# Kernel optimization log

Hardware: AMD Instinct MI355X
Metric: run time of the kernel (lower is better)

Reference implementation:

```python
import jax, jax.numpy as jnp
import numpy as np

N, E = 50000, 600000
IN_DIM, HID, HYP = 384, 128, 256
NUM_LAYERS = 3
TAU = 0.5
ALPHA = 0.1
EPS = 1e-10


def setup_inputs() -> dict:
    keys = jax.random.split(jax.random.key(0), 10)
    x = jax.random.normal(keys[0], (N, IN_DIM), dtype=jnp.float32)
    edge_index = jax.random.randint(keys[1], (2, E), 0, N, dtype=jnp.int32)
    gumbel_u = jax.random.uniform(keys[2], (N, HYP), dtype=jnp.float32, minval=1e-6, maxval=1.0 - 1e-6)
    # parameters (xavier-ish scaling)
    w_feat = jax.random.normal(keys[3], (IN_DIM, HID), dtype=jnp.float32) * np.float32(1.0 / np.sqrt(IN_DIM))
    b_feat = jnp.zeros((HID,), jnp.float32)
    w_hyper = jax.random.normal(keys[4], (HID, HYP), dtype=jnp.float32) * np.float32(np.sqrt(2.0 / (HID + HYP)))
    w_vis = jax.random.normal(keys[5], (HID, HID), dtype=jnp.float32) * np.float32(1.0 / np.sqrt(HID))
    b_vis = jnp.zeros((HID,), jnp.float32)
    w_txt = jax.random.normal(keys[6], (HID, HID), dtype=jnp.float32) * np.float32(1.0 / np.sqrt(HID))
    b_txt = jnp.zeros((HID,), jnp.float32)
    return {"x": x, "edge_index": edge_index, "gumbel_u": gumbel_u,
            "w_feat": w_feat, "b_feat": b_feat, "w_hyper": w_hyper,
            "w_vis": w_vis, "b_vis": b_vis, "w_txt": w_txt, "b_txt": b_txt}


def reference(x, edge_index, gumbel_u, w_feat, b_feat, w_hyper, w_vis, b_vis, w_txt, b_txt):
    src, dst = edge_index[0], edge_index[1]
    # LGConv gcn_norm (no self loops): deg from in-edges, norm = d_src^-1/2 * d_dst^-1/2
    deg = jax.ops.segment_sum(jnp.ones((E,), x.dtype), dst, num_segments=N)
    dinv = jnp.where(deg > 0, jnp.where(deg > 0, deg, 1.0) ** -0.5, 0.0)
    ew = dinv[src] * dinv[dst]  # [E]

    x_emb = x @ w_feat + b_feat  # [N, HID] (dropout p=0 / eval: identity)

    # stacked LightGCN propagation, mean over (num_layers+1) layer outputs
    acc = x_emb
    cur = x_emb
    for _ in range(NUM_LAYERS):
        cur = jax.ops.segment_sum(cur[src] * ew[:, None], dst, num_segments=N)
        acc = acc + cur
    local = acc / jnp.asarray(NUM_LAYERS + 1, x.dtype)

    # HGNN: gumbel-softmax soft assignment + two dense matmuls
    logits = x_emb @ w_hyper  # [N, HYP]
    g = -jnp.log(-jnp.log(gumbel_u + EPS) + EPS)
    Hm = jax.nn.softmax((logits + g) / TAU, axis=1)  # [N, HYP]
    lat = Hm.T @ x_emb            # [HYP, HID]
    hyper_out = Hm @ lat          # [N, HID]

    # F.normalize(p=2, dim=1) with eps clamp 1e-12
    nrm = jnp.maximum(jnp.linalg.norm(hyper_out, axis=1, keepdims=True), 1e-12)
    final = local + ALPHA * (hyper_out / nrm)

    x_vision = jax.nn.relu(final @ w_vis + b_vis)
    x_text = jax.nn.relu(final @ w_txt + b_txt)
    return final, x_vision, x_text
```

## Files before the change

### kernel.cpp

```cpp
#include <hip/hip_runtime.h>
#include <math.h>

#define N_NODES 50000
#define E_EDGES 600000
#define IN_DIM  384
#define HID     128
#define HYP     256

#define SCAN_NB ((N_NODES + 255) / 256)
#define EMB_NB  (N_NODES / 16)
#define DEG_NB  ((E_EDGES + 255) / 256)

#define XS_STRIDE 392

typedef __attribute__((ext_vector_type(8))) short bf16x8;
typedef __attribute__((ext_vector_type(4))) float f32x4;
typedef _Float16 f16x4 __attribute__((ext_vector_type(4)));
typedef _Float16 f16x8 __attribute__((ext_vector_type(8)));

__device__ __forceinline__ unsigned short f2bf(float f) {
    unsigned u = __builtin_bit_cast(unsigned, f);
    u = (u + 0x7FFFu + ((u >> 16) & 1u)) >> 16;
    return (unsigned short)u;
}

__device__ __forceinline__ bf16x8 cvt8(float4 p, float4 q) {
    bf16x8 a;
    a[0] = (short)f2bf(p.x); a[1] = (short)f2bf(p.y);
    a[2] = (short)f2bf(p.z); a[3] = (short)f2bf(p.w);
    a[4] = (short)f2bf(q.x); a[5] = (short)f2bf(q.y);
    a[6] = (short)f2bf(q.z); a[7] = (short)f2bf(q.w);
    return a;
}

__device__ __forceinline__ bf16x8 cvt8h(f16x8 h) {
    bf16x8 a;
#pragma unroll
    for (int i = 0; i < 8; ++i) a[i] = (short)f2bf((float)h[i]);
    return a;
}


__global__ __launch_bounds__(256) void k_scan1(const int* __restrict__ deg, int* __restrict__ bsum) {
    __shared__ int sh[256];
    int tid = threadIdx.x;
    int i = blockIdx.x * 256 + tid;
    sh[tid] = (i < N_NODES) ? deg[i] : 0;
    __syncthreads();
#pragma unroll
    for (int off = 128; off > 0; off >>= 1) {
        if (tid < off) sh[tid] += sh[tid + off];
        __syncthreads();
    }
    if (tid == 0) bsum[blockIdx.x] = sh[0];
}

__global__ __launch_bounds__(256) void k_scan2(const int* __restrict__ bsum, int* __restrict__ bbase,
                                               int* __restrict__ row_start) {
    __shared__ int sh[256];
    int tid = threadIdx.x;
    int v = (tid < SCAN_NB) ? bsum[tid] : 0;
    sh[tid] = v;
    __syncthreads();
#pragma unroll
    for (int off = 1; off < 256; off <<= 1) {
        int t = (tid >= off) ? sh[tid - off] : 0;
        __syncthreads();
        sh[tid] += t;
        __syncthreads();
    }
    if (tid < SCAN_NB) bbase[tid] = sh[tid] - v;
    if (tid == 0) row_start[N_NODES] = E_EDGES;
}

__global__ __launch_bounds__(256) void k_scan3(const int* __restrict__ deg, const int* __restrict__ bbase,
                                               int* __restrict__ row_start, float* __restrict__ dinv) {
    __shared__ int sh[256];
    int tid = threadIdx.x;
    int i = blockIdx.x * 256 + tid;
    int d = (i < N_NODES) ? deg[i] : 0;
    sh[tid] = d;
    __syncthreads();
#pragma unroll
    for (int off = 1; off < 256; off <<= 1) {
        int t = (tid >= off) ? sh[tid - off] : 0;
        __syncthreads();
        sh[tid] += t;
        __syncthreads();
    }
    if (i < N_NODES) {
        row_start[i] = sh[tid] - d + bbase[blockIdx.x];
        dinv[i] = (d > 0) ? rsqrtf((float)d) : 0.0f;
    }
}

__global__ void k_fill(const int* __restrict__ src, const int* __restrict__ dst,
                       const int* __restrict__ row_start, int* __restrict__ cnt,
                       const float* __restrict__ dinv, int2* __restrict__ csr_sw) {
    int i = blockIdx.x * blockDim.x + threadIdx.x;
    if (i < E_EDGES) {
        int d = dst[i], s = src[i];
        int pos = row_start[d] + atomicAdd(&cnt[d], 1);
        csr_sw[pos] = make_int2(s, __float_as_int(dinv[s] * dinv[d]));
    }
}


__global__ __launch_bounds__(256) void k_cvt_all(const float* __restrict__ wf, const float* __restrict__ wh,
                                                 const float* __restrict__ wv, const float* __restrict__ wt,
                                                 unsigned short* __restrict__ wfT, unsigned short* __restrict__ whT,
                                                 unsigned short* __restrict__ wvT, unsigned short* __restrict__ wtT) {
    int i = blockIdx.x * 256 + threadIdx.x;
    if (i < 49152) {
        int r = i >> 7, c = i & 127;
        wfT[(size_t)c * IN_DIM + r] = f2bf(wf[i]);
    } else if (i < 49152 + 32768) {
        int j = i - 49152;
        int r = j >> 8, c = j & 255;
        whT[(size_t)c * HID + r] = f2bf(wh[j]);
    } else if (i < 49152 + 32768 + 16384) {
        int j = i - 81920;
        int r = j >> 7, c = j & 127;
        wvT[(size_t)c * HID + r] = f2bf(wv[j]);
    } else {
        int j = i - 98304;
        int r = j >> 7, c = j & 127;
        wtT[(size_t)c * HID + r] = f2bf(wt[j]);
    }
}


__global__ __launch_bounds__(256) void k_embdeg(const float* __restrict__ x, const unsigned short* __restrict__ wfT,
                                                const float* __restrict__ bf_, _Float16* __restrict__ x_embh,
                                                const int* __restrict__ dst, int* __restrict__ deg) {
    int b = blockIdx.x;
    int tid = threadIdx.x;
    if (b >= EMB_NB) {
        int i = (b - EMB_NB) * 256 + tid;
        if (i < E_EDGES) atomicAdd(&deg[dst[i]], 1);
        return;
    }
    __shared__ unsigned short xs[16 * XS_STRIDE];
    int m0 = b * 16;
    const float* xbase = x + (size_t)m0 * IN_DIM;
#pragma unroll
    for (int pass = 0; pass < 6; ++pass) {
        int j = pass * 256 + tid;
        int row = (j * 683) >> 16;
        int col = (j - row * 96) * 4;
        float4 v = *reinterpret_cast<const float4*>(xbase + (size_t)row * IN_DIM + col);
        ushort4 sv = make_ushort4(f2bf(v.x), f2bf(v.y), f2bf(v.z), f2bf(v.w));
        *reinterpret_cast<ushort4*>(&xs[row * XS_STRIDE + col]) = sv;
    }
    __syncthreads();
    int wave = tid >> 6;
    int lane = tid & 63;
    int l16 = lane & 15, quad = lane >> 4;
    int c0 = wave * 32;
    const unsigned short* wp0 = wfT + (size_t)(c0 + l16) * IN_DIM + quad * 8;
    const unsigned short* wp1 = wp0 + (size_t)16 * IN_DIM;
    f32x4 acc0 = (f32x4){0.f, 0.f, 0.f, 0.f};
    f32x4 acc1 = (f32x4){0.f, 0.f, 0.f, 0.f};
#pragma unroll
    for (int kt = 0; kt < 12; ++kt) {
        bf16x8 a = *reinterpret_cast<const bf16x8*>(&xs[l16 * XS_STRIDE + kt * 32 + quad * 8]);
        bf16x8 b0 = *reinterpret_cast<const bf16x8*>(wp0 + kt * 32);
        bf16x8 b1 = *reinterpret_cast<const bf16x8*>(wp1 + kt * 32);
        acc0 = __builtin_amdgcn_mfma_f32_16x16x32_bf16(a, b0, acc0, 0, 0, 0);
        acc1 = __builtin_amdgcn_mfma_f32_16x16x32_bf16(a, b1, acc1, 0, 0, 0);
    }
    float bias0 = bf_[c0 + l16];
    float bias1 = bf_[c0 + 16 + l16];
#pragma unroll
    for (int r = 0; r < 4; ++r) {
        size_t row = (size_t)(m0 + quad * 4 + r);
        x_embh[row * HID + c0 + l16]      = (_Float16)(acc0[r] + bias0);
        x_embh[row * HID + c0 + 16 + l16] = (_Float16)(acc1[r] + bias1);
    }
}


__device__ __forceinline__ void fma4h(float4& a, const f16x4 v, float s) {
    a.x = fmaf((float)v.x, s, a.x);
    a.y = fmaf((float)v.y, s, a.y);
    a.z = fmaf((float)v.z, s, a.z);
    a.w = fmaf((float)v.w, s, a.w);
}

template <int INIT, int LAST>
__global__ __launch_bounds__(256) void k_prop(const _Float16* __restrict__ curh, _Float16* __restrict__ nxth,
                                              float* __restrict__ accb,
                                              const int* __restrict__ row_start,
                                              const int2* __restrict__ csr_sw) {
    int tid = threadIdx.x;
    int n = blockIdx.x * 8 + (tid >> 5);
    int c4 = (tid & 31) * 4;
    int s = row_start[n];
    int e = row_start[n + 1];
    float4 a[8];
#pragma unroll
    for (int k = 0; k < 8; ++k) a[k] = (float4){0.f, 0.f, 0.f, 0.f};
    for (int i = s; i < e; i += 8) {
        int2 pk[8];
        float wk[8];
#pragma unroll
        for (int k = 0; k < 8; ++k) {
            int j = i + k;
            pk[k] = csr_sw[(j < e) ? j : s];
            wk[k] = (j < e) ? __int_as_float(pk[k].y) : 0.0f;
        }
        f16x4 v[8];
#pragma unroll
        for (int k = 0; k < 8; ++k)
            v[k] = *reinterpret_cast<const f16x4*>(&curh[(size_t)pk[k].x * HID + c4]);
#pragma unroll
        for (int k = 0; k < 8; ++k) fma4h(a[k], v[k], wk[k]);
    }
    a[0].x += a[1].x; a[0].y += a[1].y; a[0].z += a[1].z; a[0].w += a[1].w;
    a[2].x += a[3].x; a[2].y += a[3].y; a[2].z += a[3].z; a[2].w += a[3].w;
    a[4].x += a[5].x; a[4].y += a[5].y; a[4].z += a[5].z; a[4].w += a[5].w;
    a[6].x += a[7].x; a[6].y += a[7].y; a[6].z += a[7].z; a[6].w += a[7].w;
    a[0].x += a[2].x; a[0].y += a[2].y; a[0].z += a[2].z; a[0].w += a[2].w;
    a[4].x += a[6].x; a[4].y += a[6].y; a[4].z += a[6].z; a[4].w += a[6].w;
    a[0].x += a[4].x; a[0].y += a[4].y; a[0].z += a[4].z; a[0].w += a[4].w;
    size_t o = (size_t)n * HID + c4;
    if (!LAST) {
        f16x4 oh;
        oh.x = (_Float16)a[0].x; oh.y = (_Float16)a[0].y;
        oh.z = (_Float16)a[0].z; oh.w = (_Float16)a[0].w;
        *reinterpret_cast<f16x4*>(&nxth[o]) = oh;
    }
    float4 ac;
    if (INIT) {
        f16x4 bh = *reinterpret_cast<const f16x4*>(&curh[o]);
        ac = make_float4((float)bh.x, (float)bh.y, (float)bh.z, (float)bh.w);
    } else {
        ac = *reinterpret_cast<const float4*>(&accb[o]);
    }
    ac.x += a[0].x; ac.y += a[0].y; ac.z += a[0].z; ac.w += a[0].w;
    *reinterpret_cast<float4*>(&accb[o]) = ac;
}


__global__ __launch_bounds__(64) void k_soft(const _Float16* __restrict__ x_embh,
                                             const unsigned short* __restrict__ whT,
                                             const float* __restrict__ gu, _Float16* __restrict__ Hmh) {
    int lane = threadIdx.x & 63;
    int l16 = lane & 15, quad = lane >> 4;
    int m0 = blockIdx.x * 16;
    const _Float16* xrow = x_embh + (size_t)(m0 + l16) * HID + quad * 8;
    f32x4 acc[16];
#pragma unroll
    for (int nt = 0; nt < 16; ++nt) acc[nt] = (f32x4){0.f, 0.f, 0.f, 0.f};
#pragma unroll
    for (int kt = 0; kt < HID / 32; ++kt) {
        f16x8 h = *reinterpret_cast<const f16x8*>(xrow + kt * 32);
        bf16x8 a = cvt8h(h);
#pragma unroll
        for (int nt = 0; nt < 16; ++nt) {
            bf16x8 b = *reinterpret_cast<const bf16x8*>(&whT[(size_t)(nt * 16 + l16) * HID + kt * 32 + quad * 8]);
            acc[nt] = __builtin_amdgcn_mfma_f32_16x16x32_bf16(a, b, acc[nt], 0, 0, 0);
        }
    }
#pragma unroll
    for (int nt = 0; nt < 16; ++nt) {
        int col = nt * 16 + l16;
#pragma unroll
        for (int r = 0; r < 4; ++r) {
            int row = m0 + quad * 4 + r;
            float u = gu[(size_t)row * HYP + col];
            float g = -logf(-logf(u + 1e-10f) + 1e-10f);
            acc[nt][r] = (acc[nt][r] + g) * 2.0f;
        }
    }
    float mx[4] = {-3.4e38f, -3.4e38f, -3.4e38f, -3.4e38f};
#pragma unroll
    for (int nt = 0; nt < 16; ++nt)
#pragma unroll
        for (int r = 0; r < 4; ++r) mx[r] = fmaxf(mx[r], acc[nt][r]);
#pragma unroll
    for (int r = 0; r < 4; ++r) {
        mx[r] = fmaxf(mx[r], __shfl_xor(mx[r], 1));
        mx[r] = fmaxf(mx[r], __shfl_xor(mx[r], 2));
        mx[r] = fmaxf(mx[r], __shfl_xor(mx[r], 4));
        mx[r] = fmaxf(mx[r], __shfl_xor(mx[r], 8));
    }
    float sm[4] = {0.f, 0.f, 0.f, 0.f};
#pragma unroll
    for (int nt = 0; nt < 16; ++nt)
#pragma unroll
        for (int r = 0; r < 4; ++r) {
            float e = __expf(acc[nt][r] - mx[r]);
            acc[nt][r] = e;
            sm[r] += e;
        }
#pragma unroll
    for (int r = 0; r < 4; ++r) {
        sm[r] += __shfl_xor(sm[r], 1);
        sm[r] += __shfl_xor(sm[r], 2);
        sm[r] += __shfl_xor(sm[r], 4);
        sm[r] += __shfl_xor(sm[r], 8);
        sm[r] = 1.0f / sm[r];
    }
#pragma unroll
    for (int nt = 0; nt < 16; ++nt) {
        int col = nt * 16 + l16;
#pragma unroll
        for (int r = 0; r < 4; ++r)
            Hmh[(size_t)(m0 + quad * 4 + r) * HYP + col] = (_Float16)(acc[nt][r] * sm[r]);
    }
}


#define LAT_KC 384

__global__ __launch_bounds__(256) void k_lat(const _Float16* __restrict__ Hmh, const _Float16* __restrict__ x_embh,
                                             float* __restrict__ part) {
    int htile = blockIdx.x & 1;
    int kc = blockIdx.x >> 1;
    const int chunk = (N_NODES + LAT_KC - 1) / LAT_KC;
    int start = kc * chunk;
    int end = min(N_NODES, start + chunk);
    int nn = end - start;
    int tid = threadIdx.x;
    int lh = (tid & 15) * 8;
    int d = (tid >> 4) * 8;
    const _Float16* __restrict__ hp = Hmh + (size_t)start * HYP + htile * 128 + lh;
    const _Float16* __restrict__ xp = x_embh + (size_t)start * HID + d;
    float acc[8][8];
#pragma unroll
    for (int i = 0; i < 8; ++i)
#pragma unroll
        for (int j = 0; j < 8; ++j) acc[i][j] = 0.f;
#pragma unroll 2
    for (int n = 0; n < nn; ++n) {
        f16x8 ah = *reinterpret_cast<const f16x8*>(hp);
        f16x8 bh = *reinterpret_cast<const f16x8*>(xp);
        float av[8], bv[8];
#pragma unroll
        for (int i = 0; i < 8; ++i) { av[i] = (float)ah[i]; bv[i] = (float)bh[i]; }
#pragma unroll
        for (int i = 0; i < 8; ++i)
#pragma unroll
            for (int j = 0; j < 8; ++j) acc[i][j] = fmaf(av[i], bv[j], acc[i][j]);
        hp += HYP;
        xp += HID;
    }
    float* __restrict__ pp = part + (size_t)blockIdx.x * (128 * 128) + (size_t)lh * 128 + d;
#pragma unroll
    for (int i = 0; i < 8; ++i) {
        float4 v0 = {acc[i][0], acc[i][1], acc[i][2], acc[i][3]};
        float4 v1 = {acc[i][4], acc[i][5], acc[i][6], acc[i][7]};
        *reinterpret_cast<float4*>(pp + i * 128) = v0;
        *reinterpret_cast<float4*>(pp + i * 128 + 4) = v1;
    }
}


__global__ __launch_bounds__(256) void k_lat_red(const float* __restrict__ part, unsigned short* __restrict__ latT) {
    int idx = blockIdx.x * 256 + threadIdx.x;
    int d = idx & 127;
    int h = idx >> 7;
    int htile = h >> 7;
    int lh = h & 127;
    const float* __restrict__ p0 = part + (size_t)htile * (128 * 128) + (size_t)lh * 128 + d;
    const size_t kstride = (size_t)2 * 128 * 128;
    float s0 = 0.f, s1 = 0.f, s2 = 0.f, s3 = 0.f;
#pragma unroll 4
    for (int k = 0; k < LAT_KC; k += 4) {
        s0 += p0[(size_t)k * kstride];
        s1 += p0[(size_t)(k + 1) * kstride];
        s2 += p0[(size_t)(k + 2) * kstride];
        s3 += p0[(size_t)(k + 3) * kstride];
    }
    latT[(size_t)d * HYP + h] = f2bf((s0 + s1) + (s2 + s3));
}


__global__ __launch_bounds__(64) void k_tail(const _Float16* __restrict__ Hmh, const unsigned short* __restrict__ latT,
                                             const float* __restrict__ accb,
                                             const unsigned short* __restrict__ wvT, const float* __restrict__ bv,
                                             const unsigned short* __restrict__ wtT, const float* __restrict__ bt,
                                             float* __restrict__ out_final, float* __restrict__ out_vis,
                                             float* __restrict__ out_txt) {
    __shared__ unsigned short fl[16 * HID];
    int lane = threadIdx.x & 63;
    int l16 = lane & 15, quad = lane >> 4;
    int m0 = blockIdx.x * 16;
    const _Float16* hrow = Hmh + (size_t)(m0 + l16) * HYP + quad * 8;
    f32x4 acc[8];
#pragma unroll
    for (int nt = 0; nt < 8; ++nt) acc[nt] = (f32x4){0.f, 0.f, 0.f, 0.f};
#pragma unroll
    for (int kt = 0; kt < HYP / 32; ++kt) {
        f16x8 h = *reinterpret_cast<const f16x8*>(hrow + kt * 32);
        bf16x8 a = cvt8h(h);
#pragma unroll
        for (int nt = 0; nt < 8; ++nt) {
            bf16x8 b = *reinterpret_cast<const bf16x8*>(&latT[(size_t)(nt * 16 + l16) * HYP + kt * 32 + quad * 8]);
            acc[nt] = __builtin_amdgcn_mfma_f32_16x16x32_bf16(a, b, acc[nt], 0, 0, 0);
        }
    }
    float ss[4] = {0.f, 0.f, 0.f, 0.f};
#pragma unroll
    for (int nt = 0; nt < 8; ++nt)
#pragma unroll
        for (int r = 0; r < 4; ++r) ss[r] = fmaf(acc[nt][r], acc[nt][r], ss[r]);
#pragma unroll
    for (int r = 0; r < 4; ++r) {
        ss[r] += __shfl_xor(ss[r], 1);
        ss[r] += __shfl_xor(ss[r], 2);
        ss[r] += __shfl_xor(ss[r], 4);
        ss[r] += __shfl_xor(ss[r], 8);
        ss[r] = 1.0f / fmaxf(sqrtf(ss[r]), 1e-12f);
    }
#pragma unroll
    for (int nt = 0; nt < 8; ++nt) {
        int col = nt * 16 + l16;
#pragma unroll
        for (int r = 0; r < 4; ++r) {
            int lrow = quad * 4 + r;
            size_t o = (size_t)(m0 + lrow) * HID + col;
            float f = accb[o] * 0.25f + 0.1f * (acc[nt][r] * ss[r]);
            out_final[o] = f;
            fl[lrow * HID + col] = f2bf(f);
        }
    }
    __syncthreads();
    f32x4 av[8], at4[8];
#pragma unroll
    for (int nt = 0; nt < 8; ++nt) {
        av[nt] = (f32x4){0.f, 0.f, 0.f, 0.f};
        at4[nt] = (f32x4){0.f, 0.f, 0.f, 0.f};
    }
#pragma unroll
    for (int kt = 0; kt < HID / 32; ++kt) {
        bf16x8 a = *reinterpret_cast<const bf16x8*>(&fl[l16 * HID + kt * 32 + quad * 8]);
#pragma unroll
        for (int nt = 0; nt < 8; ++nt) {
            bf16x8 b1 = *reinterpret_cast<const bf16x8*>(&wvT[(size_t)(nt * 16 + l16) * HID + kt * 32 + quad * 8]);
            bf16x8 b2 = *reinterpret_cast<const bf16x8*>(&wtT[(size_t)(nt * 16 + l16) * HID + kt * 32 + quad * 8]);
            av[nt] = __builtin_amdgcn_mfma_f32_16x16x32_bf16(a, b1, av[nt], 0, 0, 0);
            at4[nt] = __builtin_amdgcn_mfma_f32_16x16x32_bf16(a, b2, at4[nt], 0, 0, 0);
        }
    }
#pragma unroll
    for (int nt = 0; nt < 8; ++nt) {
        int col = nt * 16 + l16;
        float b1 = bv[col], b2 = bt[col];
#pragma unroll
        for (int r = 0; r < 4; ++r) {
            size_t o = (size_t)(m0 + quad * 4 + r) * HID + col;
            out_vis[o] = fmaxf(av[nt][r] + b1, 0.0f);
            out_txt[o] = fmaxf(at4[nt][r] + b2, 0.0f);
        }
    }
}


extern "C" void kernel_launch(void* const* d_in, const int* in_sizes, int n_in,
                              void* d_out, int out_size, void* d_ws, size_t ws_size,
                              hipStream_t stream) {
    const float* x      = (const float*)d_in[0];
    const int*   ei     = (const int*)d_in[1];
    const float* gu     = (const float*)d_in[2];
    const float* w_feat = (const float*)d_in[3];
    const float* b_feat = (const float*)d_in[4];
    const float* w_hyp  = (const float*)d_in[5];
    const float* w_vis  = (const float*)d_in[6];
    const float* b_vis  = (const float*)d_in[7];
    const float* w_txt  = (const float*)d_in[8];
    const float* b_txt  = (const float*)d_in[9];
    float* out = (float*)d_out;

    const int* srcv = ei;
    const int* dstv = ei + E_EDGES;

    char* p = (char*)d_ws;
    auto carve = [&p](size_t bytes) {
        char* r = p;
        p += (bytes + 63) & ~(size_t)63;
        return r;
    };
    int*      deg     = (int*)carve((size_t)N_NODES * 4);
    int*      cnt     = (int*)carve((size_t)N_NODES * 4);
    int*      rs      = (int*)carve((size_t)(N_NODES + 1) * 4);
    float*    dinv    = (float*)carve((size_t)N_NODES * 4);
    int2*     csr_sw  = (int2*)carve((size_t)E_EDGES * 8);
    _Float16* x_embh  = (_Float16*)carve((size_t)N_NODES * HID * 2);
    float*    bufA    = (float*)carve((size_t)N_NODES * HID * 4);
    float*    bufB    = (float*)carve((size_t)N_NODES * HID * 4);
    float*    accb    = (float*)carve((size_t)N_NODES * HID * 4);
    _Float16* Hmh     = (_Float16*)carve((size_t)N_NODES * HYP * 2);
    unsigned short* wfT  = (unsigned short*)carve((size_t)HID * IN_DIM * 2);
    unsigned short* whT  = (unsigned short*)carve((size_t)HYP * HID * 2);
    unsigned short* wvT  = (unsigned short*)carve((size_t)HID * HID * 2);
    unsigned short* wtT  = (unsigned short*)carve((size_t)HID * HID * 2);
    unsigned short* latT = (unsigned short*)carve((size_t)HID * HYP * 2);
    int*      bsum    = (int*)carve((size_t)SCAN_NB * 4);
    int*      bbase   = (int*)carve((size_t)SCAN_NB * 4);

    _Float16* bufAh = (_Float16*)bufA;
    _Float16* bufBh = (_Float16*)bufB;
    float* latPart = bufA;

    (void)hipMemsetAsync(d_ws, 0, (size_t)2 * N_NODES * 4 + 128, stream);

    k_cvt_all<<<448, 256, 0, stream>>>(w_feat, w_hyp, w_vis, w_txt, wfT, whT, wvT, wtT);

    k_embdeg<<<EMB_NB + DEG_NB, 256, 0, stream>>>(x, wfT, b_feat, x_embh, dstv, deg);

    k_scan1<<<SCAN_NB, 256, 0, stream>>>(deg, bsum);
    k_scan2<<<1, 256, 0, stream>>>(bsum, bbase, rs);
    k_scan3<<<SCAN_NB, 256, 0, stream>>>(deg, bbase, rs, dinv);
    k_fill<<<(E_EDGES + 255) / 256, 256, 0, stream>>>(srcv, dstv, rs, cnt, dinv, csr_sw);

    k_prop<1, 0><<<N_NODES / 8, 256, 0, stream>>>(x_embh, bufAh, accb, rs, csr_sw);
    k_prop<0, 0><<<N_NODES / 8, 256, 0, stream>>>(bufAh, bufBh, accb, rs, csr_sw);
    k_prop<0, 1><<<N_NODES / 8, 256, 0, stream>>>(bufBh, bufAh, accb, rs, csr_sw);
    k_soft<<<N_NODES / 16, 64, 0, stream>>>(x_embh, whT, gu, Hmh);
    k_lat<<<2 * LAT_KC, 256, 0, stream>>>(Hmh, x_embh, latPart);
    k_lat_red<<<(HYP * HID) / 256, 256, 0, stream>>>(latPart, latT);
    k_tail<<<N_NODES / 16, 64, 0, stream>>>(Hmh, latT, accb, wvT, b_vis, wtT, b_txt,
                                            out, out + (size_t)N_NODES * HID, out + (size_t)2 * N_NODES * HID);
}
```

Baseline: 560.3 us.

## Fuse gumbel-softmax hypergraph assignment into the embedding kernel

Moves the logits matmul, gumbel noise, and softmax that produce Hm into the embedding GEMM kernel, reusing the freshly computed x_emb tile from shared memory instead of re-reading it from global memory in a separate kernel. The 256 hyperedge columns are split across the 4 waves, and the row max and sum are reduced across waves through a small shared buffer with extra barriers. This removes one kernel launch and a pass over x_emb. In exchange the embedding kernel grows in registers and shared memory, which may reduce occupancy, and it adds the gumbel_u reads to a kernel that also runs the degree atomics.

```diff
diff --git a/kernel.cpp b/kernel.cpp
--- a/kernel.cpp
+++ b/kernel.cpp
@@ -12,6 +12,7 @@
 #define DEG_NB  ((E_EDGES + 255) / 256)
 
 #define XS_STRIDE 392
+#define XE_STRIDE 136
 
 typedef __attribute__((ext_vector_type(8))) short bf16x8;
 typedef __attribute__((ext_vector_type(4))) float f32x4;
@@ -132,6 +133,8 @@
 
 __global__ __launch_bounds__(256) void k_embdeg(const float* __restrict__ x, const unsigned short* __restrict__ wfT,
                                                 const float* __restrict__ bf_, _Float16* __restrict__ x_embh,
+                                                const unsigned short* __restrict__ whT, const float* __restrict__ gu,
+                                                _Float16* __restrict__ Hmh,
                                                 const int* __restrict__ dst, int* __restrict__ deg) {
     int b = blockIdx.x;
     int tid = threadIdx.x;
@@ -141,6 +144,8 @@
         return;
     }
     __shared__ unsigned short xs[16 * XS_STRIDE];
+    __shared__ unsigned short xe[16 * XE_STRIDE];
+    __shared__ float wred[16 * 4];
     int m0 = b * 16;
     const float* xbase = x + (size_t)m0 * IN_DIM;
 #pragma unroll
@@ -173,9 +178,96 @@
     float bias1 = bf_[c0 + 16 + l16];
 #pragma unroll
     for (int r = 0; r < 4; ++r) {
-        size_t row = (size_t)(m0 + quad * 4 + r);
-        x_embh[row * HID + c0 + l16]      = (_Float16)(acc0[r] + bias0);
-        x_embh[row * HID + c0 + 16 + l16] = (_Float16)(acc1[r] + bias1);
+        int lrow = quad * 4 + r;
+        size_t row = (size_t)(m0 + lrow);
+        float v0 = acc0[r] + bias0;
+        float v1 = acc1[r] + bias1;
+        x_embh[row * HID + c0 + l16]      = (_Float16)v0;
+        x_embh[row * HID + c0 + 16 + l16] = (_Float16)v1;
+        xe[lrow * XE_STRIDE + c0 + l16]      = f2bf(v0);
+        xe[lrow * XE_STRIDE + c0 + 16 + l16] = f2bf(v1);
+    }
+    __syncthreads();
+    f32x4 t4[4];
+#pragma unroll
+    for (int j = 0; j < 4; ++j) t4[j] = (f32x4){0.f, 0.f, 0.f, 0.f};
+#pragma unroll
+    for (int j = 0; j < 4; ++j) {
+        int nt = wave * 4 + j;
+        const unsigned short* wh = whT + (size_t)(nt * 16 + l16) * HID + quad * 8;
+#pragma unroll
+        for (int kt = 0; kt < 4; ++kt) {
+            bf16x8 a = *reinterpret_cast<const bf16x8*>(&xe[l16 * XE_STRIDE + kt * 32 + quad * 8]);
+            bf16x8 bb = *reinterpret_cast<const bf16x8*>(wh + kt * 32);
+            t4[j] = __builtin_amdgcn_mfma_f32_16x16x32_bf16(a, bb, t4[j], 0, 0, 0);
+        }
+    }
+#pragma unroll
+    for (int j = 0; j < 4; ++j) {
+        int col = (wave * 4 + j) * 16 + l16;
+#pragma unroll
+        for (int r = 0; r < 4; ++r) {
+            int row = m0 + quad * 4 + r;
+            float u = gu[(size_t)row * HYP + col];
+            float g = -logf(-logf(u + 1e-10f) + 1e-10f);
+            t4[j][r] = (t4[j][r] + g) * 2.0f;
+        }
+    }
+    float mx[4] = {-3.4e38f, -3.4e38f, -3.4e38f, -3.4e38f};
+#pragma unroll
+    for (int j = 0; j < 4; ++j)
+#pragma unroll
+        for (int r = 0; r < 4; ++r) mx[r] = fmaxf(mx[r], t4[j][r]);
+#pragma unroll
+    for (int r = 0; r < 4; ++r) {
+        mx[r] = fmaxf(mx[r], __shfl_xor(mx[r], 1));
+        mx[r] = fmaxf(mx[r], __shfl_xor(mx[r], 2));
+        mx[r] = fmaxf(mx[r], __shfl_xor(mx[r], 4));
+        mx[r] = fmaxf(mx[r], __shfl_xor(mx[r], 8));
+    }
+    if (l16 == 0) {
+#pragma unroll
+        for (int r = 0; r < 4; ++r) wred[(quad * 4 + r) * 4 + wave] = mx[r];
+    }
+    __syncthreads();
+#pragma unroll
+    for (int r = 0; r < 4; ++r) {
+        const float* wr = &wred[(quad * 4 + r) * 4];
+        mx[r] = fmaxf(fmaxf(wr[0], wr[1]), fmaxf(wr[2], wr[3]));
+    }
+    __syncthreads();
+    float sm[4] = {0.f, 0.f, 0.f, 0.f};
+#pragma unroll
+    for (int j = 0; j < 4; ++j)
+#pragma unroll
+        for (int r = 0; r < 4; ++r) {
+            float e = __expf(t4[j][r] - mx[r]);
+            t4[j][r] = e;
+            sm[r] += e;
+        }
+#pragma unroll
+    for (int r = 0; r < 4; ++r) {
+        sm[r] += __shfl_xor(sm[r], 1);
+        sm[r] += __shfl_xor(sm[r], 2);
+        sm[r] += __shfl_xor(sm[r], 4);
+        sm[r] += __shfl_xor(sm[r], 8);
+    }
+    if (l16 == 0) {
+#pragma unroll
+        for (int r = 0; r < 4; ++r) wred[(quad * 4 + r) * 4 + wave] = sm[r];
+    }
+    __syncthreads();
+#pragma unroll
+    for (int r = 0; r < 4; ++r) {
+        const float* wr = &wred[(quad * 4 + r) * 4];
+        sm[r] = 1.0f / (((wr[0] + wr[1]) + (wr[2] + wr[3])));
+    }
+#pragma unroll
+    for (int j = 0; j < 4; ++j) {
+        int col = (wave * 4 + j) * 16 + l16;
+#pragma unroll
+        for (int r = 0; r < 4; ++r)
+            Hmh[(size_t)(m0 + quad * 4 + r) * HYP + col] = (_Float16)(t4[j][r] * sm[r]);
     }
 }
 
@@ -239,76 +331,6 @@
     }
     ac.x += a[0].x; ac.y += a[0].y; ac.z += a[0].z; ac.w += a[0].w;
     *reinterpret_cast<float4*>(&accb[o]) = ac;
-}
-
-
-__global__ __launch_bounds__(64) void k_soft(const _Float16* __restrict__ x_embh,
-                                             const unsigned short* __restrict__ whT,
-                                             const float* __restrict__ gu, _Float16* __restrict__ Hmh) {
-    int lane = threadIdx.x & 63;
-    int l16 = lane & 15, quad = lane >> 4;
-    int m0 = blockIdx.x * 16;
-    const _Float16* xrow = x_embh + (size_t)(m0 + l16) * HID + quad * 8;
-    f32x4 acc[16];
-#pragma unroll
-    for (int nt = 0; nt < 16; ++nt) acc[nt] = (f32x4){0.f, 0.f, 0.f, 0.f};
-#pragma unroll
-    for (int kt = 0; kt < HID / 32; ++kt) {
-        f16x8 h = *reinterpret_cast<const f16x8*>(xrow + kt * 32);
-        bf16x8 a = cvt8h(h);
-#pragma unroll
-        for (int nt = 0; nt < 16; ++nt) {
-            bf16x8 b = *reinterpret_cast<const bf16x8*>(&whT[(size_t)(nt * 16 + l16) * HID + kt * 32 + quad * 8]);
-            acc[nt] = __builtin_amdgcn_mfma_f32_16x16x32_bf16(a, b, acc[nt], 0, 0, 0);
-        }
-    }
-#pragma unroll
-    for (int nt = 0; nt < 16; ++nt) {
-        int col = nt * 16 + l16;
-#pragma unroll
-        for (int r = 0; r < 4; ++r) {
-            int row = m0 + quad * 4 + r;
-            float u = gu[(size_t)row * HYP + col];
-            float g = -logf(-logf(u + 1e-10f) + 1e-10f);
-            acc[nt][r] = (acc[nt][r] + g) * 2.0f;
-        }
-    }
-    float mx[4] = {-3.4e38f, -3.4e38f, -3.4e38f, -3.4e38f};
-#pragma unroll
-    for (int nt = 0; nt < 16; ++nt)
-#pragma unroll
-        for (int r = 0; r < 4; ++r) mx[r] = fmaxf(mx[r], acc[nt][r]);
-#pragma unroll
-    for (int r = 0; r < 4; ++r) {
-        mx[r] = fmaxf(mx[r], __shfl_xor(mx[r], 1));
-        mx[r] = fmaxf(mx[r], __shfl_xor(mx[r], 2));
-        mx[r] = fmaxf(mx[r], __shfl_xor(mx[r], 4));
-        mx[r] = fmaxf(mx[r], __shfl_xor(mx[r], 8));
-    }
-    float sm[4] = {0.f, 0.f, 0.f, 0.f};
-#pragma unroll
-    for (int nt = 0; nt < 16; ++nt)
-#pragma unroll
-        for (int r = 0; r < 4; ++r) {
-            float e = __expf(acc[nt][r] - mx[r]);
-            acc[nt][r] = e;
-            sm[r] += e;
-        }
-#pragma unroll
-    for (int r = 0; r < 4; ++r) {
-        sm[r] += __shfl_xor(sm[r], 1);
-        sm[r] += __shfl_xor(sm[r], 2);
-        sm[r] += __shfl_xor(sm[r], 4);
-        sm[r] += __shfl_xor(sm[r], 8);
-        sm[r] = 1.0f / sm[r];
-    }
-#pragma unroll
-    for (int nt = 0; nt < 16; ++nt) {
-        int col = nt * 16 + l16;
-#pragma unroll
-        for (int r = 0; r < 4; ++r)
-            Hmh[(size_t)(m0 + quad * 4 + r) * HYP + col] = (_Float16)(acc[nt][r] * sm[r]);
-    }
 }
 
 
@@ -508,7 +530,7 @@
 
     k_cvt_all<<<448, 256, 0, stream>>>(w_feat, w_hyp, w_vis, w_txt, wfT, whT, wvT, wtT);
 
-    k_embdeg<<<EMB_NB + DEG_NB, 256, 0, stream>>>(x, wfT, b_feat, x_embh, dstv, deg);
+    k_embdeg<<<EMB_NB + DEG_NB, 256, 0, stream>>>(x, wfT, b_feat, x_embh, whT, gu, Hmh, dstv, deg);
 
     k_scan1<<<SCAN_NB, 256, 0, stream>>>(deg, bsum);
     k_scan2<<<1, 256, 0, stream>>>(bsum, bbase, rs);
@@ -518,7 +540,6 @@
     k_prop<1, 0><<<N_NODES / 8, 256, 0, stream>>>(x_embh, bufAh, accb, rs, csr_sw);
     k_prop<0, 0><<<N_NODES / 8, 256, 0, stream>>>(bufAh, bufBh, accb, rs, csr_sw);
     k_prop<0, 1><<<N_NODES / 8, 256, 0, stream>>>(bufBh, bufAh, accb, rs, csr_sw);
-    k_soft<<<N_NODES / 16, 64, 0, stream>>>(x_embh, whT, gu, Hmh);
     k_lat<<<2 * LAT_KC, 256, 0, stream>>>(Hmh, x_embh, latPart);
     k_lat_red<<<(HYP * HID) / 256, 256, 0, stream>>>(latPart, latT);
     k_tail<<<N_NODES / 16, 64, 0, stream>>>(Hmh, latT, accb, wvT, b_vis, wtT, b_txt,
```

Result: faster. 541.8 us (-3.3%).
